# Optimization experiments

Hardware: AMD Instinct MI355X
Metric: run time of the kernel (lower is better)

Reference implementation:

```python
import jax, jax.numpy as jnp
import numpy as np

B, S, D, H, E, K, V, FF, P = 1, 2048, 1024, 16, 8, 2, 32000, 4096, 4096
HD = D // H
EPS = 1e-5


def setup_inputs() -> dict:
    key = jax.random.key(0)
    ks = iter(jax.random.split(key, 64))
    w = lambda shape: jax.random.normal(next(ks), shape, jnp.float32) * 0.02
    d = {}
    d['input_ids'] = jax.random.randint(next(ks), (B, S), 0, V)
    d['embed_w'] = w((V, D))
    d['pos_w'] = w((P, D))
    for i in (0, 1):
        d[f'b{i}_ln1_g'] = jnp.ones(D); d[f'b{i}_ln1_b'] = jnp.zeros(D)
        d[f'b{i}_in_w'] = w((3 * D, D)); d[f'b{i}_in_b'] = jnp.zeros(3 * D)
        d[f'b{i}_out_w'] = w((D, D)); d[f'b{i}_out_b'] = jnp.zeros(D)
        d[f'b{i}_ln2_g'] = jnp.ones(D); d[f'b{i}_ln2_b'] = jnp.zeros(D)
    d['b0_ffn_w1'] = w((FF, D)); d['b0_ffn_b1'] = jnp.zeros(FF)
    d['b0_ffn_w2'] = w((D, FF)); d['b0_ffn_b2'] = jnp.zeros(D)
    d['b1_gate_w'] = w((E, D)); d['b1_gate_b'] = jnp.zeros(E)
    d['b1_moe_w1'] = w((E, FF, D)); d['b1_moe_b1'] = jnp.zeros((E, FF))
    d['b1_moe_w2'] = w((E, D, FF)); d['b1_moe_b2'] = jnp.zeros((E, D))
    d['norm_g'] = jnp.ones(D); d['norm_b'] = jnp.zeros(D)
    d['head_w'] = w((V, D))
    return d


def _ln(x, g, b):
    m = jnp.mean(x, -1, keepdims=True)
    v = jnp.mean(jnp.square(x - m), -1, keepdims=True)
    return (x - m) * jax.lax.rsqrt(v + EPS) * g + b


def _mha(x, in_w, in_b, out_w, out_b):
    # torch nn.MultiheadAttention (batch_first, eval mode -> no dropout)
    qkv = x @ in_w.T + in_b  # [B,S,3D]
    q, k, v = jnp.split(qkv, 3, axis=-1)
    q = q.reshape(B, S, H, HD); k = k.reshape(B, S, H, HD); v = v.reshape(B, S, H, HD)
    scores = jnp.einsum('bqhd,bkhd->bhqk', q, k) / jnp.sqrt(jnp.float32(HD))
    attn = jax.nn.softmax(scores, axis=-1)
    o = jnp.einsum('bhqk,bkhd->bqhd', attn, v).reshape(B, S, D)
    return o @ out_w.T + out_b


def _moe(h, gate_w, gate_b, w1, b1, w2, b2):
    scores = h @ gate_w.T + gate_b                       # [B,S,E]
    top_s, top_i = jax.lax.top_k(scores, K)              # [B,S,K]
    weights = jax.nn.softmax(top_s, axis=-1)             # softmax over top-k
    onehot = jax.nn.one_hot(top_i, E, dtype=h.dtype)     # [B,S,K,E]
    combine = jnp.sum(onehot * weights[..., None], axis=-2)  # [B,S,E]
    hid = jax.nn.gelu(jnp.einsum('bsd,efd->bsef', h, w1) + b1, approximate=False)
    eo = jnp.einsum('bsef,edf->bsed', hid, w2) + b2      # [B,S,E,D]
    return jnp.einsum('bsed,bse->bsd', eo, combine)


def reference(input_ids, embed_w, pos_w,
              b0_ln1_g, b0_ln1_b, b0_in_w, b0_in_b, b0_out_w, b0_out_b, b0_ln2_g, b0_ln2_b,
              b0_ffn_w1, b0_ffn_b1, b0_ffn_w2, b0_ffn_b2,
              b1_ln1_g, b1_ln1_b, b1_in_w, b1_in_b, b1_out_w, b1_out_b, b1_ln2_g, b1_ln2_b,
              b1_gate_w, b1_gate_b, b1_moe_w1, b1_moe_b1, b1_moe_w2, b1_moe_b2,
              norm_g, norm_b, head_w):
    pos = jnp.arange(S)[None, :]
    x = jnp.take(embed_w, input_ids, axis=0) + jnp.take(pos_w, pos, axis=0)
    # block 0: dense FFN
    x = x + _mha(_ln(x, b0_ln1_g, b0_ln1_b), b0_in_w, b0_in_b, b0_out_w, b0_out_b)
    h = _ln(x, b0_ln2_g, b0_ln2_b)
    ffn = jax.nn.gelu(h @ b0_ffn_w1.T + b0_ffn_b1, approximate=False) @ b0_ffn_w2.T + b0_ffn_b2
    x = x + ffn  # integration layer assumed residual add
    # block 1: MoE
    x = x + _mha(_ln(x, b1_ln1_g, b1_ln1_b), b1_in_w, b1_in_b, b1_out_w, b1_out_b)
    h = _ln(x, b1_ln2_g, b1_ln2_b)
    x = x + _moe(h, b1_gate_w, b1_gate_b, b1_moe_w1, b1_moe_b1, b1_moe_w2, b1_moe_b2)
    x = _ln(x, norm_g, norm_b)
    return x @ head_w.T
```

## Files before the change

### kernel.cpp

```cpp
#include <hip/hip_runtime.h>
#include <hip/hip_bf16.h>
#include <math.h>

typedef unsigned short ushort_t;
typedef __attribute__((ext_vector_type(8))) __bf16 bf16x8;
typedef __attribute__((ext_vector_type(4))) float f32x4;
typedef __attribute__((ext_vector_type(8))) short s8v;
typedef __attribute__((ext_vector_type(4))) short s4v;

#define SQ 2048
#define DM 1024
#define NH 16
#define HDIM 64
#define FFD 4096
#define NVOC 32000

__device__ inline float b2f(unsigned short u) {
  union { unsigned int i; float f; } x; x.i = ((unsigned int)u) << 16; return x.f;
}
__device__ inline unsigned short f2b(float f) {
  __hip_bfloat16 h = __float2bfloat16(f);
  return *reinterpret_cast<unsigned short*>(&h);
}
__device__ inline void split2(float x, ushort_t& h, ushort_t& l) {
  h = f2b(x);
  l = f2b(x - b2f(h));
}
__device__ inline float geluf(float v) {
  return 0.5f * v * (1.0f + erff(v * 0.70710678118654752f));
}
__device__ __forceinline__ void gld16(const void* g, void* l) {
  __builtin_amdgcn_global_load_lds(
      (const __attribute__((address_space(1))) void*)g,
      (__attribute__((address_space(3))) void*)l, 16, 0, 0);
}
#define MFMA __builtin_amdgcn_mfma_f32_16x16x32_bf16

template<int EPI, int NT, int KS>
__device__ __forceinline__ void gemmsp_body(
    const ushort_t* __restrict__ AH, const ushort_t* __restrict__ AL,
    int lda, long long bA,
    const ushort_t* __restrict__ BH, const ushort_t* __restrict__ BL,
    int ldb, long long bB,
    float* __restrict__ C, ushort_t* __restrict__ CH, ushort_t* __restrict__ CL,
    int ldc, long long bC, long long pC,
    int M, int N, int K, const float* __restrict__ bias, float alpha)
{
  int z = blockIdx.z, h = z / KS, kc = z % KS;
  const ushort_t* AHp = AH + (long long)h * bA + (long long)kc * K;
  const ushort_t* ALp = AL + (long long)h * bA + (long long)kc * K;
  const ushort_t* BHp = BH + (long long)h * bB + (long long)kc * K;
  const ushort_t* BLp = BL + (long long)h * bB + (long long)kc * K;
  int m0 = blockIdx.x * 128, n0 = blockIdx.y * NT;
  const int NF = NT / 32;

  __shared__ __align__(16) ushort_t sAH[128 * 32], sAL[128 * 32];
  __shared__ __align__(16) ushort_t sBH[NT * 32],  sBL[NT * 32];

  int tid = threadIdx.x, lane = tid & 63, wave = tid >> 6;
  int wr = (wave >> 1) * 64, wc = (wave & 1) * (NT >> 1);
  int l15 = lane & 15, l4 = lane >> 4;

  f32x4 acc[4][NF];
#pragma unroll
  for (int m = 0; m < 4; ++m)
#pragma unroll
    for (int n = 0; n < NF; ++n) acc[m][n] = (f32x4){0.f, 0.f, 0.f, 0.f};

  for (int k0 = 0; k0 < K; k0 += 32) {
#pragma unroll
    for (int i = 0; i < 2; ++i) {
      int fi = i * 2048 + tid * 8;
      int r = fi >> 5, chk = (fi >> 3) & 3;
      int scol = ((chk ^ ((r >> 1) & 3)) << 3);
      int ra = m0 + r; if (ra > M - 1) ra = M - 1;
      long long go = (long long)ra * lda + k0 + scol;
      gld16(AHp + go, &sAH[fi]);
      gld16(ALp + go, &sAL[fi]);
    }
#pragma unroll
    for (int i = 0; i < NT / 64; ++i) {
      int fi = i * 2048 + tid * 8;
      int r = fi >> 5, chk = (fi >> 3) & 3;
      int scol = ((chk ^ ((r >> 1) & 3)) << 3);
      int rb = n0 + r; if (rb > N - 1) rb = N - 1;
      long long go = (long long)rb * ldb + k0 + scol;
      gld16(BHp + go, &sBH[fi]);
      gld16(BLp + go, &sBL[fi]);
    }
    __syncthreads();
    bf16x8 ah[4], al[4], bh[NF], bl[NF];
#pragma unroll
    for (int m = 0; m < 4; ++m) {
      int r = wr + m * 16 + l15;
      int o = r * 32 + ((l4 ^ ((r >> 1) & 3)) << 3);
      ah[m] = *(const bf16x8*)&sAH[o];
      al[m] = *(const bf16x8*)&sAL[o];
    }
#pragma unroll
    for (int n = 0; n < NF; ++n) {
      int r = wc + n * 16 + l15;
      int o = r * 32 + ((l4 ^ ((r >> 1) & 3)) << 3);
      bh[n] = *(const bf16x8*)&sBH[o];
      bl[n] = *(const bf16x8*)&sBL[o];
    }
#pragma unroll
    for (int m = 0; m < 4; ++m)
#pragma unroll
      for (int n = 0; n < NF; ++n) {
        acc[m][n] = MFMA(ah[m], bh[n], acc[m][n], 0, 0, 0);
        acc[m][n] = MFMA(al[m], bh[n], acc[m][n], 0, 0, 0);
        acc[m][n] = MFMA(ah[m], bl[n], acc[m][n], 0, 0, 0);
      }
    __syncthreads();
  }

#pragma unroll
  for (int m = 0; m < 4; ++m) {
#pragma unroll
    for (int n = 0; n < NF; ++n) {
      int c = n0 + wc + n * 16 + l15;
      if (c >= N) continue;
      float bv = (EPI == 0 || EPI == 3 || EPI == 4) ? bias[c] : 0.f;
#pragma unroll
      for (int q = 0; q < 4; ++q) {
        int rr = m0 + wr + m * 16 + l4 * 4 + q;
        if (rr >= M) continue;
        float v = acc[m][n][q];
        if (EPI == 0) {
          ushort_t hh, ll; split2(v + bv, hh, ll);
          long long o = (long long)rr * ldc + c; CH[o] = hh; CL[o] = ll;
        } else if (EPI == 3) {
          C[(long long)rr * ldc + c] += v + bv;
        } else if (EPI == 4) {
          ushort_t hh, ll; split2(geluf(v + bv), hh, ll);
          long long o = (long long)rr * ldc + c; CH[o] = hh; CL[o] = ll;
        }
      }
    }
  }
}

#define SP_ARGS const ushort_t* AH, const ushort_t* AL, int lda, long long bA, \
    const ushort_t* BH, const ushort_t* BL, int ldb, long long bB, \
    float* C, ushort_t* CH, ushort_t* CL, int ldc, long long bC, long long pC, \
    int M, int N, int K, const float* bias, float alpha
#define SP_PASS AH, AL, lda, bA, BH, BL, ldb, bB, C, CH, CL, ldc, bC, pC, M, N, K, bias, alpha

__global__ __launch_bounds__(256) void k_qkv (SP_ARGS) { gemmsp_body<0,128,1>(SP_PASS); }
__global__ __launch_bounds__(256) void k_outp(SP_ARGS) { gemmsp_body<3, 64,1>(SP_PASS); }
__global__ __launch_bounds__(256) void k_ffn1(SP_ARGS) { gemmsp_body<4,128,1>(SP_PASS); }
__global__ __launch_bounds__(256) void k_ffn2(SP_ARGS) { gemmsp_body<3, 64,1>(SP_PASS); }

__global__ __launch_bounds__(256)
void k_attn(const ushort_t* __restrict__ qkvH, const ushort_t* __restrict__ qkvL,
            const ushort_t* __restrict__ VtH, const ushort_t* __restrict__ VtL,
            ushort_t* __restrict__ aH, ushort_t* __restrict__ aL)
{
  int q0 = blockIdx.x * 64;
  int h  = blockIdx.y;
  __shared__ __align__(16) ushort_t sQH[4096], sQL[4096];
  __shared__ __align__(16) ushort_t sKH[4096], sKL[4096];
  __shared__ __align__(16) ushort_t sVH[4096], sVL[4096];
  __shared__ __align__(16) ushort_t sPH[4096], sPL[4096];

  int tid = threadIdx.x, lane = tid & 63, wave = tid >> 6;
  int l15 = lane & 15, l4 = lane >> 4;

#pragma unroll
  for (int i = 0; i < 2; ++i) {
    int idx = i * 2048 + tid * 8;
    int row = idx >> 6, chk = (idx >> 3) & 7;
    int scol = ((chk ^ (row & 7)) << 3);
    long long go = (long long)(q0 + row) * (3 * DM) + h * 64 + scol;
    gld16(qkvH + go, &sQH[idx]);
    gld16(qkvL + go, &sQL[idx]);
  }

  float mrow[4], lrow[4];
  f32x4 Oacc[4];
#pragma unroll
  for (int r = 0; r < 4; ++r) { mrow[r] = -1e30f; lrow[r] = 0.f; }
#pragma unroll
  for (int n = 0; n < 4; ++n) Oacc[n] = (f32x4){0.f, 0.f, 0.f, 0.f};

  for (int kt = 0; kt < SQ / 64; ++kt) {
#pragma unroll
    for (int i = 0; i < 2; ++i) {
      int idx = i * 2048 + tid * 8;
      int row = idx >> 6, chk = (idx >> 3) & 7;
      int scol = ((chk ^ (row & 7)) << 3);
      long long gk = (long long)(kt * 64 + row) * (3 * DM) + DM + h * 64 + scol;
      long long gv = (long long)(h * 64 + row) * SQ + kt * 64 + scol;
      gld16(qkvH + gk, &sKH[idx]);
      gld16(qkvL + gk, &sKL[idx]);
      gld16(VtH + gv, &sVH[idx]);
      gld16(VtL + gv, &sVL[idx]);
    }
    __syncthreads();

    f32x4 S[4];
#pragma unroll
    for (int n = 0; n < 4; ++n) S[n] = (f32x4){0.f, 0.f, 0.f, 0.f};
#pragma unroll
    for (int kk = 0; kk < 64; kk += 32) {
      int ar = wave * 16 + l15;
      int ao = ar * 64 + ((((kk >> 3) + l4) ^ (ar & 7)) << 3);
      bf16x8 qh = *(const bf16x8*)&sQH[ao];
      bf16x8 ql = *(const bf16x8*)&sQL[ao];
#pragma unroll
      for (int n = 0; n < 4; ++n) {
        int br = n * 16 + l15;
        int bo = br * 64 + ((((kk >> 3) + l4) ^ (br & 7)) << 3);
        bf16x8 kh = *(const bf16x8*)&sKH[bo];
        bf16x8 kl = *(const bf16x8*)&sKL[bo];
        S[n] = MFMA(qh, kh, S[n], 0, 0, 0);
        S[n] = MFMA(ql, kh, S[n], 0, 0, 0);
        S[n] = MFMA(qh, kl, S[n], 0, 0, 0);
      }
    }
    float tm[4], ts[4];
#pragma unroll
    for (int r = 0; r < 4; ++r) {
#pragma unroll
      for (int n = 0; n < 4; ++n) S[n][r] *= 0.125f;
      tm[r] = fmaxf(fmaxf(S[0][r], S[1][r]), fmaxf(S[2][r], S[3][r]));
    }
#pragma unroll
    for (int mk = 1; mk <= 8; mk <<= 1)
#pragma unroll
      for (int r = 0; r < 4; ++r) tm[r] = fmaxf(tm[r], __shfl_xor(tm[r], mk));
#pragma unroll
    for (int r = 0; r < 4; ++r) {
      float mn = fmaxf(mrow[r], tm[r]);
      float corr = __expf(mrow[r] - mn);
      mrow[r] = mn;
      float s = 0.f;
#pragma unroll
      for (int n = 0; n < 4; ++n) { S[n][r] = __expf(S[n][r] - mn); s += S[n][r]; }
      ts[r] = s;
      lrow[r] *= corr;
#pragma unroll
      for (int n = 0; n < 4; ++n) Oacc[n][r] *= corr;
    }
#pragma unroll
    for (int mk = 1; mk <= 8; mk <<= 1)
#pragma unroll
      for (int r = 0; r < 4; ++r) ts[r] += __shfl_xor(ts[r], mk);
#pragma unroll
    for (int r = 0; r < 4; ++r) lrow[r] += ts[r];

    {
      ushort_t* pH = &sPH[wave * 1024];
      ushort_t* pL = &sPL[wave * 1024];
#pragma unroll
      for (int n = 0; n < 4; ++n)
#pragma unroll
        for (int r = 0; r < 4; ++r) {
          int row = l4 * 4 + r, col = n * 16 + l15;
          int ad = row * 64 + (((col >> 3) ^ (row & 7)) << 3) + (col & 7);
          ushort_t hh, ll; split2(S[n][r], hh, ll);
          pH[ad] = hh; pL[ad] = ll;
        }
    }
    __syncthreads();
#pragma unroll
    for (int kk = 0; kk < 64; kk += 32) {
      int ao = wave * 1024 + l15 * 64 + ((((kk >> 3) + l4) ^ (l15 & 7)) << 3);
      bf16x8 ph = *(const bf16x8*)&sPH[ao];
      bf16x8 pl = *(const bf16x8*)&sPL[ao];
#pragma unroll
      for (int n = 0; n < 4; ++n) {
        int br = n * 16 + l15;
        int bo = br * 64 + ((((kk >> 3) + l4) ^ (br & 7)) << 3);
        bf16x8 vh = *(const bf16x8*)&sVH[bo];
        bf16x8 vl = *(const bf16x8*)&sVL[bo];
        Oacc[n] = MFMA(ph, vh, Oacc[n], 0, 0, 0);
        Oacc[n] = MFMA(pl, vh, Oacc[n], 0, 0, 0);
        Oacc[n] = MFMA(ph, vl, Oacc[n], 0, 0, 0);
      }
    }
    __syncthreads();
  }

#pragma unroll
  for (int n = 0; n < 4; ++n)
#pragma unroll
    for (int r = 0; r < 4; ++r) {
      int q = q0 + wave * 16 + l4 * 4 + r;
      int d = h * 64 + n * 16 + l15;
      float val = Oacc[n][r] / lrow[r];
      ushort_t hh, ll; split2(val, hh, ll);
      long long o = (long long)q * DM + d;
      aH[o] = hh; aL[o] = ll;
    }
}

template<int EPI, int BSRC, int SWAP, int KS, int XS>
__device__ __forceinline__ void gemm16_body(
    const ushort_t* __restrict__ A, int lda, long long bA,
    const void* __restrict__ Bv, int ldb, long long bB,
    void* __restrict__ Cv, int ldc, long long bC, long long pC,
    int M, int N, int K, const float* __restrict__ bias, int bBias,
    const int* __restrict__ offs)
{
  int bz = blockIdx.z;
  int z = bz / KS, kc = bz % KS;
  int Kc = K / KS;
  const ushort_t* Ap = A + (long long)z * bA + (long long)kc * Kc;
  int rowStart = 0, Meff = M;
  if (offs) { rowStart = offs[z]; Meff = offs[z + 1] - rowStart; }
  int bx = blockIdx.x, by = blockIdx.y;
  if (XS) {
    int flat = bx + by * gridDim.x;
    int cpx = (gridDim.x * gridDim.y) >> 3;
    int s = (flat & 7) * cpx + (flat >> 3);
    bx = s % gridDim.x; by = s / gridDim.x;
  }
  int m0 = (SWAP ? by : bx) * 128;
  if (m0 >= Meff) return;
  int n0 = (SWAP ? bx : by) * 128;

  __shared__ __align__(16) ushort_t As[128 * 64];
  __shared__ __align__(16) ushort_t Bs[128 * 64];

  int tid = threadIdx.x, lane = tid & 63, wave = tid >> 6;
  int wr = (wave >> 1) * 64, wc = (wave & 1) * 64;
  int l15 = lane & 15, l4 = lane >> 4;

  f32x4 acc[4][4];
#pragma unroll
  for (int m = 0; m < 4; ++m)
#pragma unroll
    for (int n = 0; n < 4; ++n) acc[m][n] = (f32x4){0.f, 0.f, 0.f, 0.f};

  for (int k0 = 0; k0 < Kc; k0 += 64) {
#pragma unroll
    for (int i = 0; i < 4; ++i) {
      int idx = i * 2048 + tid * 8;
      int row = idx >> 6, chk = (idx >> 3) & 7;
      int scol = ((chk ^ (row & 7)) << 3);
      int ra = m0 + row; if (ra > Meff - 1) ra = Meff - 1;
      gld16(Ap + (long long)(rowStart + ra) * lda + k0 + scol, &As[idx]);
    }
    if (BSRC == 1) {
      const ushort_t* Bp = (const ushort_t*)Bv + (long long)z * bB + (long long)kc * Kc;
#pragma unroll
      for (int i = 0; i < 4; ++i) {
        int idx = i * 2048 + tid * 8;
        int row = idx >> 6, chk = (idx >> 3) & 7;
        int scol = ((chk ^ (row & 7)) << 3);
        int rb = n0 + row; if (rb > N - 1) rb = N - 1;
        gld16(Bp + (long long)rb * ldb + k0 + scol, &Bs[idx]);
      }
    } else {
      const float* Bf = (const float*)Bv + (long long)z * bB + (long long)kc * Kc;
#pragma unroll
      for (int i = 0; i < 8; ++i) {
        int g = tid + i * 256;
        int r = g >> 4, c4 = (g & 15) * 4;
        int rb = n0 + r; if (rb > N - 1) rb = N - 1;
        float4 f = *(const float4*)(Bf + (long long)rb * ldb + k0 + c4);
        s4v o; o[0] = (short)f2b(f.x); o[1] = (short)f2b(f.y);
        o[2] = (short)f2b(f.z); o[3] = (short)f2b(f.w);
        int dst = r * 64 + (((c4 >> 3) ^ (r & 7)) << 3) + (c4 & 7);
        *(s4v*)&Bs[dst] = o;
      }
    }
    __syncthreads();
#pragma unroll
    for (int kk = 0; kk < 64; kk += 32) {
      bf16x8 af[4], bfr[4];
#pragma unroll
      for (int m = 0; m < 4; ++m) {
        int r = wr + m * 16 + l15;
        af[m] = *(const bf16x8*)&As[r * 64 + ((((kk >> 3) + l4) ^ (r & 7)) << 3)];
      }
#pragma unroll
      for (int n = 0; n < 4; ++n) {
        int r = wc + n * 16 + l15;
        bfr[n] = *(const bf16x8*)&Bs[r * 64 + ((((kk >> 3) + l4) ^ (r & 7)) << 3)];
      }
#pragma unroll
      for (int m = 0; m < 4; ++m)
#pragma unroll
        for (int n = 0; n < 4; ++n)
          acc[m][n] = MFMA(af[m], bfr[n], acc[m][n], 0, 0, 0);
    }
    __syncthreads();
  }

#pragma unroll
  for (int m = 0; m < 4; ++m) {
#pragma unroll
    for (int n = 0; n < 4; ++n) {
      int c = n0 + wc + n * 16 + l15;
      if (c >= N) continue;
      float bv = (EPI == 2) ? bias[(long long)z * bBias + c] : 0.f;
#pragma unroll
      for (int q = 0; q < 4; ++q) {
        int rr = m0 + wr + m * 16 + l4 * 4 + q;
        if (rr >= Meff) continue;
        float v = acc[m][n][q];
        long long crow = rowStart + rr;
        if (EPI == 2)
          ((ushort_t*)Cv)[crow * ldc + (long long)z * bC + c] = f2b(geluf(v + bv));
        else if (EPI == 6)
          ((float*)Cv)[crow * ldc + c] = v;
        else if (EPI == 7)
          ((float*)Cv)[(long long)kc * pC + crow * ldc + c] = v;
      }
    }
  }
}

#define G16_ARGS const ushort_t* A, int lda, long long bA, const void* Bv, \
    int ldb, long long bB, void* Cv, int ldc, long long bC, long long pC, \
    int M, int N, int K, const float* bias, int bBias, const int* offs
#define G16_PASS A, lda, bA, Bv, ldb, bB, Cv, ldc, bC, pC, M, N, K, bias, bBias, offs

__global__ __launch_bounds__(256) void k_moe1   (G16_ARGS) { gemm16_body<2,1,1,1,0>(G16_PASS); }
__global__ __launch_bounds__(256) void k_moe2   (G16_ARGS) { gemm16_body<7,1,1,2,0>(G16_PASS); }
__global__ __launch_bounds__(256) void k_head_bf(G16_ARGS) { gemm16_body<6,1,0,1,1>(G16_PASS); }
__global__ __launch_bounds__(256) void k_head_f (G16_ARGS) { gemm16_body<6,0,0,1,1>(G16_PASS); }

__global__ __launch_bounds__(256)
void cvt_split(const float* __restrict__ s, ushort_t* __restrict__ dh,
               ushort_t* __restrict__ dl, int n4)
{
  int i = blockIdx.x * blockDim.x + threadIdx.x;
  int stride = gridDim.x * blockDim.x;
  for (; i < n4; i += stride) {
    float4 f = ((const float4*)s)[i];
    s4v h, l; ushort_t hh, ll;
    split2(f.x, hh, ll); h[0] = (short)hh; l[0] = (short)ll;
    split2(f.y, hh, ll); h[1] = (short)hh; l[1] = (short)ll;
    split2(f.z, hh, ll); h[2] = (short)hh; l[2] = (short)ll;
    split2(f.w, hh, ll); h[3] = (short)hh; l[3] = (short)ll;
    ((s4v*)dh)[i] = h; ((s4v*)dl)[i] = l;
  }
}

__global__ __launch_bounds__(256)
void cvt_bf16(const float* __restrict__ s, ushort_t* __restrict__ d, int n4)
{
  int i = blockIdx.x * blockDim.x + threadIdx.x;
  int stride = gridDim.x * blockDim.x;
  for (; i < n4; i += stride) {
    float4 f = ((const float4*)s)[i];
    s4v o; o[0] = (short)f2b(f.x); o[1] = (short)f2b(f.y);
    o[2] = (short)f2b(f.z); o[3] = (short)f2b(f.w);
    ((s4v*)d)[i] = o;
  }
}

__global__ __launch_bounds__(256)
void embed_kernel(const int* __restrict__ ids, const float* __restrict__ ew,
                  const float* __restrict__ pw, float* __restrict__ x)
{
  int srow = blockIdx.x, tid = threadIdx.x;
  int id = ids[srow];
  const float4 e = *(const float4*)(ew + (long long)id * DM + tid * 4);
  const float4 p = *(const float4*)(pw + (long long)srow * DM + tid * 4);
  float4* xr = (float4*)(x + (long long)srow * DM) + tid;
  *xr = make_float4(e.x + p.x, e.y + p.y, e.z + p.z, e.w + p.w);
}

template<int MODE>
__global__ __launch_bounds__(256)
void ln_kernel(const float* __restrict__ x, const float* __restrict__ g,
               const float* __restrict__ b, ushort_t* __restrict__ outH,
               ushort_t* __restrict__ outL)
{
  int row = blockIdx.x, tid = threadIdx.x;
  float4 v = ((const float4*)(x + (long long)row * DM))[tid];
  __shared__ float sm1[4], sm2[4];
  float s = v.x + v.y + v.z + v.w;
  for (int o = 32; o > 0; o >>= 1) s += __shfl_down(s, o);
  if ((tid & 63) == 0) sm1[tid >> 6] = s;
  __syncthreads();
  float mean = (sm1[0] + sm1[1] + sm1[2] + sm1[3]) * (1.0f / DM);
  float d0 = v.x - mean, d1 = v.y - mean, d2 = v.z - mean, d3 = v.w - mean;
  float q = d0 * d0 + d1 * d1 + d2 * d2 + d3 * d3;
  for (int o = 32; o > 0; o >>= 1) q += __shfl_down(q, o);
  if ((tid & 63) == 0) sm2[tid >> 6] = q;
  __syncthreads();
  float var = (sm2[0] + sm2[1] + sm2[2] + sm2[3]) * (1.0f / DM);
  float rstd = rsqrtf(var + 1e-5f);
  float4 gv = ((const float4*)g)[tid];
  float4 bv = ((const float4*)b)[tid];
  float o0 = d0 * rstd * gv.x + bv.x, o1 = d1 * rstd * gv.y + bv.y;
  float o2 = d2 * rstd * gv.z + bv.z, o3 = d3 * rstd * gv.w + bv.w;
  long long base = (long long)row * DM + tid * 4;
  if (MODE == 0) {
    ushort_t hh, ll;
    split2(o0, hh, ll); outH[base + 0] = hh; outL[base + 0] = ll;
    split2(o1, hh, ll); outH[base + 1] = hh; outL[base + 1] = ll;
    split2(o2, hh, ll); outH[base + 2] = hh; outL[base + 2] = ll;
    split2(o3, hh, ll); outH[base + 3] = hh; outL[base + 3] = ll;
  } else {
    outH[base + 0] = f2b(o0); outH[base + 1] = f2b(o1);
    outH[base + 2] = f2b(o2); outH[base + 3] = f2b(o3);
  }
}

__global__ __launch_bounds__(256)
void transpose_v2(const ushort_t* __restrict__ qH, const ushort_t* __restrict__ qL,
                  ushort_t* __restrict__ vH, ushort_t* __restrict__ vL)
{
  __shared__ ushort_t tH[64][65], tL[64][65];
  int j0 = blockIdx.x * 64, h = blockIdx.y;
  int tid = threadIdx.x;
  int jr = tid >> 2, d0 = (tid & 3) * 16;
  long long so = (long long)(j0 + jr) * (3 * DM) + 2 * DM + h * 64 + d0;
#pragma unroll
  for (int i = 0; i < 16; ++i) { tH[jr][d0 + i] = qH[so + i]; tL[jr][d0 + i] = qL[so + i]; }
  __syncthreads();
  int dd = tid >> 2, jc = (tid & 3) * 16;
  long long dofs = (long long)(h * 64 + dd) * SQ + j0 + jc;
#pragma unroll
  for (int i = 0; i < 16; ++i) { vH[dofs + i] = tH[jc + i][dd]; vL[dofs + i] = tL[jc + i][dd]; }
}

__global__ __launch_bounds__(256)
void ln_gate_top2(const float* __restrict__ x, const float* __restrict__ g,
                  const float* __restrict__ b, const float* __restrict__ gw,
                  const float* __restrict__ gb, int* __restrict__ topi,
                  float* __restrict__ topw, int* __restrict__ counts)
{
  int row = blockIdx.x, tid = threadIdx.x;
  float4 v = ((const float4*)(x + (long long)row * DM))[tid];
  __shared__ float sm1[4], sm2[4];
  __shared__ float se[8][4];
  float s = v.x + v.y + v.z + v.w;
  for (int o = 32; o > 0; o >>= 1) s += __shfl_down(s, o);
  if ((tid & 63) == 0) sm1[tid >> 6] = s;
  __syncthreads();
  float mean = (sm1[0] + sm1[1] + sm1[2] + sm1[3]) * (1.0f / DM);
  float d0 = v.x - mean, d1 = v.y - mean, d2 = v.z - mean, d3 = v.w - mean;
  float q = d0 * d0 + d1 * d1 + d2 * d2 + d3 * d3;
  for (int o = 32; o > 0; o >>= 1) q += __shfl_down(q, o);
  if ((tid & 63) == 0) sm2[tid >> 6] = q;
  __syncthreads();
  float var = (sm2[0] + sm2[1] + sm2[2] + sm2[3]) * (1.0f / DM);
  float rstd = rsqrtf(var + 1e-5f);
  float4 gv = ((const float4*)g)[tid];
  float4 bv = ((const float4*)b)[tid];
  float h0 = d0 * rstd * gv.x + bv.x, h1 = d1 * rstd * gv.y + bv.y;
  float h2 = d2 * rstd * gv.z + bv.z, h3 = d3 * rstd * gv.w + bv.w;
#pragma unroll
  for (int e = 0; e < 8; ++e) {
    float4 w = ((const float4*)(gw + (long long)e * DM))[tid];
    float p = h0 * w.x + h1 * w.y + h2 * w.z + h3 * w.w;
    for (int o = 32; o > 0; o >>= 1) p += __shfl_down(p, o);
    if ((tid & 63) == 0) se[e][tid >> 6] = p;
  }
  __syncthreads();
  if (tid == 0) {
    float sc[8];
#pragma unroll
    for (int e = 0; e < 8; ++e)
      sc[e] = se[e][0] + se[e][1] + se[e][2] + se[e][3] + gb[e];
    int i1 = 0; float m1 = sc[0];
    for (int e = 1; e < 8; ++e) if (sc[e] > m1) { m1 = sc[e]; i1 = e; }
    int i2 = -1; float m2 = -1e30f;
    for (int e = 0; e < 8; ++e) if (e != i1 && sc[e] > m2) { m2 = sc[e]; i2 = e; }
    float e2 = __expf(m2 - m1);
    float w1 = 1.f / (1.f + e2);
    topi[row * 2] = i1; topi[row * 2 + 1] = i2;
    topw[row * 2] = w1; topw[row * 2 + 1] = 1.f - w1;
    atomicAdd(&counts[i1], 1);
    atomicAdd(&counts[i2], 1);
  }
}

__global__ void moe_zero(int* counts) { if (threadIdx.x < 8) counts[threadIdx.x] = 0; }

__global__ void moe_prefix(const int* __restrict__ counts, int* __restrict__ offs,
                           int* __restrict__ cursors)
{
  if (threadIdx.x == 0 && blockIdx.x == 0) {
    int a = 0;
    for (int e = 0; e < 8; ++e) { offs[e] = a; a += counts[e]; cursors[e] = 0; }
    offs[8] = a;
  }
}

__global__ __launch_bounds__(256)
void moe_gather(const ushort_t* __restrict__ hH, const int* __restrict__ topi,
                const float* __restrict__ topw, const int* __restrict__ offs,
                int* __restrict__ cursors, int* __restrict__ tokIdx,
                float* __restrict__ tokW, int* __restrict__ slotOf,
                ushort_t* __restrict__ Xg)
{
  int tok = blockIdx.x, tid = threadIdx.x;
  __shared__ int s0s, s1s;
  if (tid == 0) {
    int e0 = topi[tok * 2], e1 = topi[tok * 2 + 1];
    int s0 = offs[e0] + atomicAdd(&cursors[e0], 1);
    int s1 = offs[e1] + atomicAdd(&cursors[e1], 1);
    tokIdx[s0] = tok; tokW[s0] = topw[tok * 2];
    tokIdx[s1] = tok; tokW[s1] = topw[tok * 2 + 1];
    slotOf[tok * 2] = s0; slotOf[tok * 2 + 1] = s1;
    s0s = s0; s1s = s1;
  }
  __syncthreads();
  s4v v = ((const s4v*)(hH + (long long)tok * DM))[tid];
  ((s4v*)(Xg + (long long)s0s * DM))[tid] = v;
  ((s4v*)(Xg + (long long)s1s * DM))[tid] = v;
}

__global__ __launch_bounds__(256)
void moe_reduce(float* __restrict__ x, const float* __restrict__ eo, long long pC,
                const int* __restrict__ slotOf, const int* __restrict__ topi,
                const float* __restrict__ topw, const float* __restrict__ b2)
{
  int tok = blockIdx.x, tid = threadIdx.x;
  int s0 = slotOf[tok * 2], s1 = slotOf[tok * 2 + 1];
  int e0 = topi[tok * 2], e1 = topi[tok * 2 + 1];
  float w0 = topw[tok * 2], w1 = topw[tok * 2 + 1];
  float4 a  = ((const float4*)(eo + (long long)s0 * DM))[tid];
  float4 a2 = ((const float4*)(eo + pC + (long long)s0 * DM))[tid];
  float4 b  = ((const float4*)(eo + (long long)s1 * DM))[tid];
  float4 b2v= ((const float4*)(eo + pC + (long long)s1 * DM))[tid];
  float4 ba = ((const float4*)(b2 + (long long)e0 * DM))[tid];
  float4 bb = ((const float4*)(b2 + (long long)e1 * DM))[tid];
  float4* xr = (float4*)(x + (long long)tok * DM) + tid;
  float4 xv = *xr;
  xv.x += w0 * (a.x + a2.x + ba.x) + w1 * (b.x + b2v.x + bb.x);
  xv.y += w0 * (a.y + a2.y + ba.y) + w1 * (b.y + b2v.y + bb.y);
  xv.z += w0 * (a.z + a2.z + ba.z) + w1 * (b.z + b2v.z + bb.z);
  xv.w += w0 * (a.w + a2.w + ba.w) + w1 * (b.w + b2v.w + bb.w);
  *xr = xv;
}

extern "C" void kernel_launch(void* const* d_in, const int* in_sizes, int n_in,
                              void* d_out, int out_size, void* d_ws, size_t ws_size,
                              hipStream_t stream)
{
  const int* ids = (const int*)d_in[0];
  const float* embed_w = (const float*)d_in[1];
  const float* pos_w   = (const float*)d_in[2];
  const float* ln1_g[2] = {(const float*)d_in[3],  (const float*)d_in[11]};
  const float* ln1_b[2] = {(const float*)d_in[4],  (const float*)d_in[12]};
  const float* in_w[2]  = {(const float*)d_in[5],  (const float*)d_in[13]};
  const float* in_b[2]  = {(const float*)d_in[6],  (const float*)d_in[14]};
  const float* out_w[2] = {(const float*)d_in[7],  (const float*)d_in[15]};
  const float* out_b[2] = {(const float*)d_in[8],  (const float*)d_in[16]};
  const float* ln2_g[2] = {(const float*)d_in[9],  (const float*)d_in[17]};
  const float* ln2_b[2] = {(const float*)d_in[10], (const float*)d_in[18]};
  const float* ffn_w1 = (const float*)d_in[19];
  const float* ffn_b1 = (const float*)d_in[20];
  const float* ffn_w2 = (const float*)d_in[21];
  const float* ffn_b2 = (const float*)d_in[22];
  const float* gate_w = (const float*)d_in[23];
  const float* gate_b = (const float*)d_in[24];
  const float* moe_w1 = (const float*)d_in[25];
  const float* moe_b1 = (const float*)d_in[26];
  const float* moe_w2 = (const float*)d_in[27];
  const float* moe_b2 = (const float*)d_in[28];
  const float* norm_g = (const float*)d_in[29];
  const float* norm_b = (const float*)d_in[30];
  const float* head_w = (const float*)d_in[31];

  char* ob = (char*)d_out;
  size_t off = 0;
  auto alloc = [&](size_t bytes) {
    char* p = ob + off;
    off = (off + bytes + 255) & ~(size_t)255;
    return p;
  };
  float*    x      = (float*)alloc((size_t)SQ * DM * 4);
  ushort_t* hbufH  = (ushort_t*)alloc((size_t)SQ * DM * 2);
  ushort_t* hbufL  = (ushort_t*)alloc((size_t)SQ * DM * 2);
  ushort_t* qkvH   = (ushort_t*)alloc((size_t)SQ * 3 * DM * 2);
  ushort_t* qkvL   = (ushort_t*)alloc((size_t)SQ * 3 * DM * 2);
  ushort_t* VtH    = (ushort_t*)alloc((size_t)NH * HDIM * SQ * 2);
  ushort_t* VtL    = (ushort_t*)alloc((size_t)NH * HDIM * SQ * 2);
  char*     resv   = (char*)alloc((size_t)32 << 20);
  ushort_t* attnH  = (ushort_t*)alloc((size_t)SQ * DM * 2);
  ushort_t* attnL  = (ushort_t*)alloc((size_t)SQ * DM * 2);
  ushort_t* Xg     = (ushort_t*)alloc((size_t)2 * SQ * DM * 2);
  int*      topi   = (int*)alloc(SQ * 2 * 4);
  float*    topw   = (float*)alloc(SQ * 2 * 4);
  int*      tokIdx = (int*)alloc(2 * SQ * 4);
  float*    tokW   = (float*)alloc(2 * SQ * 4);
  int*      slotOf = (int*)alloc(2 * SQ * 4);
  int*      counts = (int*)alloc(256);
  int*      offsb  = (int*)alloc(256);
  int*      cursors= (int*)alloc(256);
  ushort_t* ffnH   = (ushort_t*)alloc((size_t)SQ * FFD * 2);
  ushort_t* ffnL   = (ushort_t*)alloc((size_t)SQ * FFD * 2);
  float*    eo     = (float*)alloc((size_t)2 * 2 * SQ * DM * 4);
  ushort_t* inwH[2], *inwL[2], *outwH[2], *outwL[2];
  ushort_t* wsplit0 = (ushort_t*)alloc(0);
  inwH[0]  = (ushort_t*)alloc((size_t)3 * DM * DM * 2);
  inwL[0]  = (ushort_t*)alloc((size_t)3 * DM * DM * 2);
  inwH[1]  = (ushort_t*)alloc((size_t)3 * DM * DM * 2);
  inwL[1]  = (ushort_t*)alloc((size_t)3 * DM * DM * 2);
  outwH[0] = (ushort_t*)alloc((size_t)DM * DM * 2);
  outwL[0] = (ushort_t*)alloc((size_t)DM * DM * 2);
  outwH[1] = (ushort_t*)alloc((size_t)DM * DM * 2);
  outwL[1] = (ushort_t*)alloc((size_t)DM * DM * 2);
  ushort_t* f1H = (ushort_t*)alloc((size_t)FFD * DM * 2);
  ushort_t* f1L = (ushort_t*)alloc((size_t)FFD * DM * 2);
  ushort_t* f2H = (ushort_t*)alloc((size_t)DM * FFD * 2);
  ushort_t* f2L = (ushort_t*)alloc((size_t)DM * FFD * 2);
  ushort_t* moe_w1b = wsplit0;
  ushort_t* moe_w2b = qkvH;
  ushort_t* moehid  = ffnH;
  const long long eoPC = (long long)2 * SQ * DM;
  ushort_t* hfin    = (ushort_t*)d_ws;
  bool wsBig = ws_size >= ((size_t)70 << 20);
  ushort_t* head_wb = (ushort_t*)((char*)d_ws + ((size_t)4 << 20));
  (void)resv;

  moe_zero<<<1, 64, 0, stream>>>(counts);
  embed_kernel<<<SQ, 256, 0, stream>>>(ids, embed_w, pos_w, x);
  cvt_split<<<512, 256, 0, stream>>>(in_w[0], inwH[0], inwL[0], 3 * DM * DM / 4);
  cvt_split<<<512, 256, 0, stream>>>(in_w[1], inwH[1], inwL[1], 3 * DM * DM / 4);
  cvt_split<<<512, 256, 0, stream>>>(out_w[0], outwH[0], outwL[0], DM * DM / 4);
  cvt_split<<<512, 256, 0, stream>>>(out_w[1], outwH[1], outwL[1], DM * DM / 4);
  cvt_split<<<512, 256, 0, stream>>>(ffn_w1, f1H, f1L, FFD * DM / 4);
  cvt_split<<<512, 256, 0, stream>>>(ffn_w2, f2H, f2L, DM * FFD / 4);
  if (wsBig)
    cvt_bf16<<<1024, 256, 0, stream>>>(head_w, head_wb, NVOC * DM / 4);

  for (int L = 0; L < 2; ++L) {
    ln_kernel<0><<<SQ, 256, 0, stream>>>(x, ln1_g[L], ln1_b[L], hbufH, hbufL);
    k_qkv<<<dim3(16, 24, 1), 256, 0, stream>>>(
        hbufH, hbufL, DM, 0, inwH[L], inwL[L], DM, 0,
        nullptr, qkvH, qkvL, 3 * DM, 0, 0,
        SQ, 3 * DM, DM, in_b[L], 1.f);
    transpose_v2<<<dim3(SQ / 64, NH), 256, 0, stream>>>(qkvH, qkvL, VtH, VtL);
    k_attn<<<dim3(SQ / 64, NH), 256, 0, stream>>>(qkvH, qkvL, VtH, VtL,
                                                  attnH, attnL);
    k_outp<<<dim3(16, 16, 1), 256, 0, stream>>>(
        attnH, attnL, DM, 0, outwH[L], outwL[L], DM, 0,
        x, nullptr, nullptr, DM, 0, 0,
        SQ, DM, DM, out_b[L], 1.f);
    if (L == 0) {
      ln_kernel<0><<<SQ, 256, 0, stream>>>(x, ln2_g[0], ln2_b[0], hbufH, hbufL);
      k_ffn1<<<dim3(16, 32, 1), 256, 0, stream>>>(
          hbufH, hbufL, DM, 0, f1H, f1L, DM, 0,
          nullptr, ffnH, ffnL, FFD, 0, 0,
          SQ, FFD, DM, ffn_b1, 1.f);
      k_ffn2<<<dim3(16, 16, 1), 256, 0, stream>>>(
          ffnH, ffnL, FFD, 0, f2H, f2L, FFD, 0,
          x, nullptr, nullptr, DM, 0, 0,
          SQ, DM, FFD, ffn_b2, 1.f);
    } else {
      cvt_bf16<<<2048, 256, 0, stream>>>(moe_w1, moe_w1b, 8 * FFD * DM / 4);
      cvt_bf16<<<2048, 256, 0, stream>>>(moe_w2, moe_w2b, 8 * DM * FFD / 4);
      ln_gate_top2<<<SQ, 256, 0, stream>>>(x, ln2_g[1], ln2_b[1], gate_w, gate_b,
                                           topi, topw, counts);
      moe_prefix<<<1, 64, 0, stream>>>(counts, offsb, cursors);
      ln_kernel<1><<<SQ, 256, 0, stream>>>(x, ln2_g[1], ln2_b[1], hbufH, nullptr);
      moe_gather<<<SQ, 256, 0, stream>>>(hbufH, topi, topw, offsb, cursors,
                                         tokIdx, tokW, slotOf, Xg);
      k_moe1<<<dim3(32, 16, 8), 256, 0, stream>>>(
          Xg, DM, 0, moe_w1b, DM, (long long)FFD * DM,
          moehid, FFD, 0, 0, SQ, FFD, DM, moe_b1, FFD, offsb);
      k_moe2<<<dim3(8, 16, 16), 256, 0, stream>>>(
          moehid, FFD, 0, moe_w2b, FFD, (long long)DM * FFD,
          eo, DM, 0, eoPC, SQ, DM, FFD, nullptr, 0, offsb);
      moe_reduce<<<SQ, 256, 0, stream>>>(x, eo, eoPC, slotOf, topi, topw, moe_b2);
    }
  }
  ln_kernel<1><<<SQ, 256, 0, stream>>>(x, norm_g, norm_b, hfin, nullptr);
  if (wsBig)
    k_head_bf<<<dim3(16, 250, 1), 256, 0, stream>>>(
        hfin, DM, 0, head_wb, DM, 0, d_out, NVOC, 0, 0,
        SQ, NVOC, DM, nullptr, 0, nullptr);
  else
    k_head_f<<<dim3(16, 250, 1), 256, 0, stream>>>(
        hfin, DM, 0, head_w, DM, 0, d_out, NVOC, 0, 0,
        SQ, NVOC, DM, nullptr, 0, nullptr);
}
```

Measured before the change: 1.336 ms.

## Keep Q in registers, swizzle attention grid, stage fp32 GEMM epilogue via LDS, fuse LN

```diff
diff --git a/kernel.cpp b/kernel.cpp
--- a/kernel.cpp
+++ b/kernel.cpp
@@ -157,9 +157,11 @@
             const ushort_t* __restrict__ VtH, const ushort_t* __restrict__ VtL,
             ushort_t* __restrict__ aH, ushort_t* __restrict__ aL)
 {
-  int q0 = blockIdx.x * 64;
-  int h  = blockIdx.y;
-  __shared__ __align__(16) ushort_t sQH[4096], sQL[4096];
+  int f = blockIdx.x + blockIdx.y * gridDim.x;
+  int logical = (f & 7) * 64 + (f >> 3);
+  int q0 = (logical & 31) * 64;
+  int h  = logical >> 5;
+
   __shared__ __align__(16) ushort_t sKH[4096], sKL[4096];
   __shared__ __align__(16) ushort_t sVH[4096], sVL[4096];
   __shared__ __align__(16) ushort_t sPH[4096], sPL[4096];
@@ -167,14 +169,13 @@
   int tid = threadIdx.x, lane = tid & 63, wave = tid >> 6;
   int l15 = lane & 15, l4 = lane >> 4;
 
-#pragma unroll
-  for (int i = 0; i < 2; ++i) {
-    int idx = i * 2048 + tid * 8;
-    int row = idx >> 6, chk = (idx >> 3) & 7;
-    int scol = ((chk ^ (row & 7)) << 3);
-    long long go = (long long)(q0 + row) * (3 * DM) + h * 64 + scol;
-    gld16(qkvH + go, &sQH[idx]);
-    gld16(qkvL + go, &sQL[idx]);
+  bf16x8 qh[2], ql[2];
+  {
+    long long base = (long long)(q0 + wave * 16 + l15) * (3 * DM) + h * 64 + l4 * 8;
+    qh[0] = *(const bf16x8*)(qkvH + base);
+    qh[1] = *(const bf16x8*)(qkvH + base + 32);
+    ql[0] = *(const bf16x8*)(qkvL + base);
+    ql[1] = *(const bf16x8*)(qkvL + base + 32);
   }
 
   float mrow[4], lrow[4];
@@ -204,19 +205,17 @@
     for (int n = 0; n < 4; ++n) S[n] = (f32x4){0.f, 0.f, 0.f, 0.f};
 #pragma unroll
     for (int kk = 0; kk < 64; kk += 32) {
-      int ar = wave * 16 + l15;
-      int ao = ar * 64 + ((((kk >> 3) + l4) ^ (ar & 7)) << 3);
-      bf16x8 qh = *(const bf16x8*)&sQH[ao];
-      bf16x8 ql = *(const bf16x8*)&sQL[ao];
+      int kkI = kk >> 5;
+      bf16x8 qhf = qh[kkI], qlf = ql[kkI];
 #pragma unroll
       for (int n = 0; n < 4; ++n) {
         int br = n * 16 + l15;
         int bo = br * 64 + ((((kk >> 3) + l4) ^ (br & 7)) << 3);
         bf16x8 kh = *(const bf16x8*)&sKH[bo];
         bf16x8 kl = *(const bf16x8*)&sKL[bo];
-        S[n] = MFMA(qh, kh, S[n], 0, 0, 0);
-        S[n] = MFMA(ql, kh, S[n], 0, 0, 0);
-        S[n] = MFMA(qh, kl, S[n], 0, 0, 0);
+        S[n] = MFMA(qhf, kh, S[n], 0, 0, 0);
+        S[n] = MFMA(qlf, kh, S[n], 0, 0, 0);
+        S[n] = MFMA(qhf, kl, S[n], 0, 0, 0);
       }
     }
     float tm[4], ts[4];
@@ -321,8 +320,9 @@
   if (m0 >= Meff) return;
   int n0 = (SWAP ? bx : by) * 128;
 
-  __shared__ __align__(16) ushort_t As[128 * 64];
-  __shared__ __align__(16) ushort_t Bs[128 * 64];
+  __shared__ __align__(16) char smem[32768];
+  ushort_t* As = (ushort_t*)smem;
+  ushort_t* Bs = (ushort_t*)(smem + 16384);
 
   int tid = threadIdx.x, lane = tid & 63, wave = tid >> 6;
   int wr = (wave >> 1) * 64, wc = (wave & 1) * 64;
@@ -360,9 +360,9 @@
         int g = tid + i * 256;
         int r = g >> 4, c4 = (g & 15) * 4;
         int rb = n0 + r; if (rb > N - 1) rb = N - 1;
-        float4 f = *(const float4*)(Bf + (long long)rb * ldb + k0 + c4);
-        s4v o; o[0] = (short)f2b(f.x); o[1] = (short)f2b(f.y);
-        o[2] = (short)f2b(f.z); o[3] = (short)f2b(f.w);
+        float4 fv = *(const float4*)(Bf + (long long)rb * ldb + k0 + c4);
+        s4v o; o[0] = (short)f2b(fv.x); o[1] = (short)f2b(fv.y);
+        o[2] = (short)f2b(fv.z); o[3] = (short)f2b(fv.w);
         int dst = r * 64 + (((c4 >> 3) ^ (r & 7)) << 3) + (c4 & 7);
         *(s4v*)&Bs[dst] = o;
       }
@@ -388,6 +388,38 @@
           acc[m][n] = MFMA(af[m], bfr[n], acc[m][n], 0, 0, 0);
     }
     __syncthreads();
+  }
+
+  if (EPI == 6 || EPI == 7) {
+    float* fE = (float*)smem;
+#pragma unroll
+    for (int h2 = 0; h2 < 2; ++h2) {
+      if ((wave >> 1) == h2) {
+#pragma unroll
+        for (int m = 0; m < 4; ++m)
+#pragma unroll
+          for (int n = 0; n < 4; ++n)
+#pragma unroll
+            for (int q = 0; q < 4; ++q)
+              fE[(m * 16 + l4 * 4 + q) * 128 + wc + n * 16 + l15] = acc[m][n][q];
+      }
+      __syncthreads();
+#pragma unroll
+      for (int i = 0; i < 8; ++i) {
+        int lin = tid + i * 256;
+        int row = lin >> 5, c4 = (lin & 31) << 2;
+        int gr = m0 + h2 * 64 + row;
+        if (gr < Meff) {
+          float4 v4 = *(const float4*)&fE[row * 128 + c4];
+          long long crow = rowStart + gr;
+          float* dst = (float*)Cv + (EPI == 7 ? (long long)kc * pC : 0LL)
+                       + crow * ldc + n0 + c4;
+          *(float4*)dst = v4;
+        }
+      }
+      __syncthreads();
+    }
+    return;
   }
 
 #pragma unroll
@@ -405,10 +437,6 @@
         long long crow = rowStart + rr;
         if (EPI == 2)
           ((ushort_t*)Cv)[crow * ldc + (long long)z * bC + c] = f2b(geluf(v + bv));
-        else if (EPI == 6)
-          ((float*)Cv)[crow * ldc + c] = v;
-        else if (EPI == 7)
-          ((float*)Cv)[(long long)kc * pC + crow * ldc + c] = v;
       }
     }
   }
@@ -526,7 +554,8 @@
 void ln_gate_top2(const float* __restrict__ x, const float* __restrict__ g,
                   const float* __restrict__ b, const float* __restrict__ gw,
                   const float* __restrict__ gb, int* __restrict__ topi,
-                  float* __restrict__ topw, int* __restrict__ counts)
+                  float* __restrict__ topw, int* __restrict__ counts,
+                  ushort_t* __restrict__ outH)
 {
   int row = blockIdx.x, tid = threadIdx.x;
   float4 v = ((const float4*)(x + (long long)row * DM))[tid];
@@ -548,6 +577,9 @@
   float4 bv = ((const float4*)b)[tid];
   float h0 = d0 * rstd * gv.x + bv.x, h1 = d1 * rstd * gv.y + bv.y;
   float h2 = d2 * rstd * gv.z + bv.z, h3 = d3 * rstd * gv.w + bv.w;
+  long long base = (long long)row * DM + tid * 4;
+  outH[base + 0] = f2b(h0); outH[base + 1] = f2b(h1);
+  outH[base + 2] = f2b(h2); outH[base + 3] = f2b(h3);
 #pragma unroll
   for (int e = 0; e < 8; ++e) {
     float4 w = ((const float4*)(gw + (long long)e * DM))[tid];
@@ -753,9 +785,8 @@
       cvt_bf16<<<2048, 256, 0, stream>>>(moe_w1, moe_w1b, 8 * FFD * DM / 4);
       cvt_bf16<<<2048, 256, 0, stream>>>(moe_w2, moe_w2b, 8 * DM * FFD / 4);
       ln_gate_top2<<<SQ, 256, 0, stream>>>(x, ln2_g[1], ln2_b[1], gate_w, gate_b,
-                                           topi, topw, counts);
+                                           topi, topw, counts, hbufH);
       moe_prefix<<<1, 64, 0, stream>>>(counts, offsb, cursors);
-      ln_kernel<1><<<SQ, 256, 0, stream>>>(x, ln2_g[1], ln2_b[1], hbufH, nullptr);
       moe_gather<<<SQ, 256, 0, stream>>>(hbufH, topi, topw, offsb, cursors,
                                          tokIdx, tokW, slotOf, Xg);
       k_moe1<<<dim3(32, 16, 8), 256, 0, stream>>>(
```

After: 1.332 ms. No clear change (-0.3%).
